# Optimization experiments

Hardware: AMD Instinct MI355X
Metric: run time of the kernel (lower is better)

## Reference

```python
import jax, jax.numpy as jnp
import numpy as np

H, W, D = 160, 160, 16
VOXEL_SIZE = 0.4
VOL_MIN = np.array([-32.0, -32.0, -1.0], dtype=np.float32)
SCALE_MULTIPLIER = 3.0
N_GAUSS = 8192
CHUNK = 64


def setup_inputs() -> dict:
    key = jax.random.key(0)
    k1, k2, k3, k4, k5 = jax.random.split(key, 5)
    vol_min = jnp.asarray(VOL_MIN)
    vol_ext = jnp.array([64.0, 64.0, 6.4], dtype=jnp.float32)
    means3d = jax.random.uniform(k1, (N_GAUSS, 3), jnp.float32) * vol_ext + vol_min
    opacities = jax.random.uniform(k2, (N_GAUSS, 1), jnp.float32)
    # per-axis std devs: 0.2..0.8 m so 3-sigma footprint spans a handful of voxels
    scales = 0.2 + 0.6 * jax.random.uniform(k3, (N_GAUSS, 3), jnp.float32)
    rotations = jax.random.normal(k4, (N_GAUSS, 4), jnp.float32)
    features = jax.random.normal(k5, (N_GAUSS, 32), jnp.float32)
    return {"means3d": means3d, "opacities": opacities, "scales": scales,
            "rotations": rotations, "features": features}


def quat_to_rotmat(q):
    # q: [N,4] wxyz, normalized
    w, x, y, z = q[:, 0], q[:, 1], q[:, 2], q[:, 3]
    R = jnp.stack([
        jnp.stack([1 - 2 * (y * y + z * z), 2 * (x * y - w * z), 2 * (x * z + w * y)], -1),
        jnp.stack([2 * (x * y + w * z), 1 - 2 * (x * x + z * z), 2 * (y * z - w * x)], -1),
        jnp.stack([2 * (x * z - w * y), 2 * (y * z + w * x), 1 - 2 * (x * x + y * y)], -1),
    ], axis=-2)  # [N,3,3]
    return R


def _grid_coords():
    ii, jj, kk = jnp.meshgrid(jnp.arange(H), jnp.arange(W), jnp.arange(D), indexing="ij")
    idx = jnp.stack([ii, jj, kk], axis=-1).astype(jnp.float32)
    return (idx + 0.5) * VOXEL_SIZE + jnp.asarray(VOL_MIN)  # [H,W,D,3] voxel centers


def reference(means3d, opacities, scales, rotations, features):
    x = _grid_coords().reshape(-1, 3)  # [V,3]
    q = rotations / jnp.linalg.norm(rotations, axis=-1, keepdims=True)
    R = quat_to_rotmat(q)
    # covariance = R diag(s^2) R^T
    cov = jnp.einsum("nij,nj,nkj->nik", R, scales * scales, R)
    cov_inv = jnp.linalg.inv(cov)
    sigma = jnp.sqrt(jnp.diagonal(cov, axis1=1, axis2=2))  # [N,3]
    opac = opacities[:, 0]  # [N]
    n = means3d.shape[0]
    nchunks = n // CHUNK

    def chunked(a):
        return a.reshape(nchunks, CHUNK, *a.shape[1:])

    def step(acc, c):
        mu, op, sg, ci, ft = c
        diff = x[:, None, :] - mu[None, :, :]  # [V,CHUNK,3]
        maha = jnp.einsum("vci,cij,vcj->vc", diff, ci, diff)
        # local aggregation cutoff: within scale_multiplier * sigma box around mean
        mask = jnp.all(jnp.abs(diff) <= SCALE_MULTIPLIER * sg[None, :, :], axis=-1)
        w = op[None, :] * jnp.exp(-0.5 * maha) * mask  # [V,CHUNK]
        return acc + w @ ft, None

    acc0 = jnp.zeros((x.shape[0], features.shape[-1]), jnp.float32)
    xs = (chunked(means3d), chunked(opac), chunked(sigma), chunked(cov_inv), chunked(features))
    acc, _ = jax.lax.scan(step, acc0, xs)
    return acc.reshape(H, W, D, features.shape[-1])
```

## Files before the change

kernel.cpp:

```cpp
#include <hip/hip_runtime.h>

#define HH 160
#define WW 160
#define DD 16
#define NG 8192
#define VOXEL 0.4f

#define TTX 20
#define TTY 20
#define TTZ 4
#define NTILES (TTX * TTY * TTZ)
#define CAP 128


__global__ __launch_bounds__(64) void gv_precompute_bin(
    const float* __restrict__ means, const float* __restrict__ opac,
    const float* __restrict__ scales, const float* __restrict__ rots,
    const float4* __restrict__ feats, int* __restrict__ tileCnt,
    float4* __restrict__ tileData) {
  int g = blockIdx.x * 64 + threadIdx.x;
  if (g >= NG) return;
  float qw = rots[g * 4 + 0], qx = rots[g * 4 + 1];
  float qy = rots[g * 4 + 2], qz = rots[g * 4 + 3];
  float inv = rsqrtf(qw * qw + qx * qx + qy * qy + qz * qz);
  qw *= inv; qx *= inv; qy *= inv; qz *= inv;
  float R[3][3];
  R[0][0] = 1.f - 2.f * (qy * qy + qz * qz);
  R[0][1] = 2.f * (qx * qy - qw * qz);
  R[0][2] = 2.f * (qx * qz + qw * qy);
  R[1][0] = 2.f * (qx * qy + qw * qz);
  R[1][1] = 1.f - 2.f * (qx * qx + qz * qz);
  R[1][2] = 2.f * (qy * qz - qw * qx);
  R[2][0] = 2.f * (qx * qz - qw * qy);
  R[2][1] = 2.f * (qy * qz + qw * qx);
  R[2][2] = 1.f - 2.f * (qx * qx + qy * qy);
  float sx = scales[g * 3 + 0], sy = scales[g * 3 + 1], sz = scales[g * 3 + 2];
  float s2[3] = {sx * sx, sy * sy, sz * sz};
  float is2[3] = {1.f / s2[0], 1.f / s2[1], 1.f / s2[2]};
  float cov00 = 0.f, cov11 = 0.f, cov22 = 0.f;
  float ci00 = 0.f, ci01 = 0.f, ci02 = 0.f, ci11 = 0.f, ci12 = 0.f, ci22 = 0.f;
#pragma unroll
  for (int c = 0; c < 3; c++) {
    cov00 += R[0][c] * R[0][c] * s2[c];
    cov11 += R[1][c] * R[1][c] * s2[c];
    cov22 += R[2][c] * R[2][c] * s2[c];
    ci00 += R[0][c] * R[0][c] * is2[c];
    ci01 += R[0][c] * R[1][c] * is2[c];
    ci02 += R[0][c] * R[2][c] * is2[c];
    ci11 += R[1][c] * R[1][c] * is2[c];
    ci12 += R[1][c] * R[2][c] * is2[c];
    ci22 += R[2][c] * R[2][c] * is2[c];
  }
  float mx = means[g * 3 + 0], my = means[g * 3 + 1], mz = means[g * 3 + 2];
  float bx = 3.f * sqrtf(cov00), by = 3.f * sqrtf(cov11), bz = 3.f * sqrtf(cov22);

  const float eps = 1e-4f;
  int i0 = (int)ceilf((mx - bx + 32.f) * 2.5f - 0.5f - eps);
  int i1 = (int)floorf((mx + bx + 32.f) * 2.5f - 0.5f + eps);
  int j0 = (int)ceilf((my - by + 32.f) * 2.5f - 0.5f - eps);
  int j1 = (int)floorf((my + by + 32.f) * 2.5f - 0.5f + eps);
  int k0 = (int)ceilf((mz - bz + 1.f) * 2.5f - 0.5f - eps);
  int k1 = (int)floorf((mz + bz + 1.f) * 2.5f - 0.5f + eps);
  i0 = max(i0, 0); i1 = min(i1, HH - 1);
  j0 = max(j0, 0); j1 = min(j1, WW - 1);
  k0 = max(k0, 0); k1 = min(k1, DD - 1);
  if (i0 > i1 || j0 > j1 || k0 > k1) return;

  float4 p0 = make_float4(mx, my, mz, opac[g]);
  float4 p1 = make_float4(bx, by, bz, ci00);
  float4 p2 = make_float4(ci01, ci02, ci11, ci12);
  float4 p3 = make_float4(ci22, 0.f, 0.f, 0.f);
  const float4* __restrict__ fsrc = feats + (size_t)g * 8;
  float4 f0 = fsrc[0], f1 = fsrc[1], f2 = fsrc[2], f3 = fsrc[3];
  float4 f4 = fsrc[4], f5 = fsrc[5], f6 = fsrc[6], f7 = fsrc[7];

  int ti0 = i0 >> 3, ti1 = i1 >> 3;
  int tj0 = j0 >> 3, tj1 = j1 >> 3;
  int tk0 = k0 >> 2, tk1 = k1 >> 2;
  for (int ti = ti0; ti <= ti1; ti++)
    for (int tj = tj0; tj <= tj1; tj++)
      for (int tk = tk0; tk <= tk1; tk++) {
        int t = (ti * TTY + tj) * TTZ + tk;
        int pos = atomicAdd(&tileCnt[t], 1);
        if (pos < CAP) {
          float4* __restrict__ d = tileData + ((size_t)t * CAP + pos) * 12;
          d[0] = p0;  d[1] = p1;  d[2] = p2;  d[3] = p3;
          d[4] = f0;  d[5] = f1;  d[6] = f2;  d[7] = f3;
          d[8] = f4;  d[9] = f5;  d[10] = f6; d[11] = f7;
        }
      }
}

__global__ __launch_bounds__(256) void gv_voxelize(
    const int* __restrict__ tileCnt, const float4* __restrict__ tileData,
    float4* __restrict__ out) {
  int tid = threadIdx.x;
  int dk = tid & 3, dj = (tid >> 2) & 7, di = tid >> 5;
  int tk = blockIdx.x, tj = blockIdx.y, ti = blockIdx.z;
  int i = ti * 8 + di, j = tj * 8 + dj, k = tk * 4 + dk;

  float px = (i + 0.5f) * VOXEL - 32.f;
  float py = (j + 0.5f) * VOXEL - 32.f;
  float pz = (k + 0.5f) * VOXEL - 1.f;

  int t = (ti * TTY + tj) * TTZ + tk;
  int cnt = tileCnt[t];
  cnt = min(cnt, CAP);
  const float4* __restrict__ gd = tileData + (size_t)t * CAP * 12;

  float4 acc[8];
#pragma unroll
  for (int f = 0; f < 8; f++) acc[f] = make_float4(0.f, 0.f, 0.f, 0.f);

  int n = 0;
  for (; n + 2 <= cnt; n += 2) {
    const float4* __restrict__ q0 = gd + (size_t)n * 12;
    const float4* __restrict__ q1 = q0 + 12;
    float4 a0 = q0[0], b0 = q0[1], c0 = q0[2], d0 = q0[3];
    float4 e00 = q0[4], e01 = q0[5], e02 = q0[6], e03 = q0[7];
    float4 e04 = q0[8], e05 = q0[9], e06 = q0[10], e07 = q0[11];
    float4 a1 = q1[0], b1 = q1[1], c1 = q1[2], d1 = q1[3];
    float4 e10 = q1[4], e11 = q1[5], e12 = q1[6], e13 = q1[7];
    float4 e14 = q1[8], e15 = q1[9], e16 = q1[10], e17 = q1[11];

    float dx0 = px - a0.x, dy0 = py - a0.y, dz0 = pz - a0.z;
    float dx1 = px - a1.x, dy1 = py - a1.y, dz1 = pz - a1.z;
    bool in0 = (fabsf(dx0) <= b0.x) & (fabsf(dy0) <= b0.y) & (fabsf(dz0) <= b0.z);
    bool in1 = (fabsf(dx1) <= b1.x) & (fabsf(dy1) <= b1.y) & (fabsf(dz1) <= b1.z);

    if (__any(in0)) {
      float maha = b0.w * dx0 * dx0 + c0.z * dy0 * dy0 + d0.x * dz0 * dz0 +
                   2.f * (c0.x * dx0 * dy0 + c0.y * dx0 * dz0 + c0.w * dy0 * dz0);
      float wgt = in0 ? a0.w * __expf(-0.5f * maha) : 0.f;
      acc[0].x += wgt * e00.x; acc[0].y += wgt * e00.y; acc[0].z += wgt * e00.z; acc[0].w += wgt * e00.w;
      acc[1].x += wgt * e01.x; acc[1].y += wgt * e01.y; acc[1].z += wgt * e01.z; acc[1].w += wgt * e01.w;
      acc[2].x += wgt * e02.x; acc[2].y += wgt * e02.y; acc[2].z += wgt * e02.z; acc[2].w += wgt * e02.w;
      acc[3].x += wgt * e03.x; acc[3].y += wgt * e03.y; acc[3].z += wgt * e03.z; acc[3].w += wgt * e03.w;
      acc[4].x += wgt * e04.x; acc[4].y += wgt * e04.y; acc[4].z += wgt * e04.z; acc[4].w += wgt * e04.w;
      acc[5].x += wgt * e05.x; acc[5].y += wgt * e05.y; acc[5].z += wgt * e05.z; acc[5].w += wgt * e05.w;
      acc[6].x += wgt * e06.x; acc[6].y += wgt * e06.y; acc[6].z += wgt * e06.z; acc[6].w += wgt * e06.w;
      acc[7].x += wgt * e07.x; acc[7].y += wgt * e07.y; acc[7].z += wgt * e07.z; acc[7].w += wgt * e07.w;
    }
    if (__any(in1)) {
      float maha = b1.w * dx1 * dx1 + c1.z * dy1 * dy1 + d1.x * dz1 * dz1 +
                   2.f * (c1.x * dx1 * dy1 + c1.y * dx1 * dz1 + c1.w * dy1 * dz1);
      float wgt = in1 ? a1.w * __expf(-0.5f * maha) : 0.f;
      acc[0].x += wgt * e10.x; acc[0].y += wgt * e10.y; acc[0].z += wgt * e10.z; acc[0].w += wgt * e10.w;
      acc[1].x += wgt * e11.x; acc[1].y += wgt * e11.y; acc[1].z += wgt * e11.z; acc[1].w += wgt * e11.w;
      acc[2].x += wgt * e12.x; acc[2].y += wgt * e12.y; acc[2].z += wgt * e12.z; acc[2].w += wgt * e12.w;
      acc[3].x += wgt * e13.x; acc[3].y += wgt * e13.y; acc[3].z += wgt * e13.z; acc[3].w += wgt * e13.w;
      acc[4].x += wgt * e14.x; acc[4].y += wgt * e14.y; acc[4].z += wgt * e14.z; acc[4].w += wgt * e14.w;
      acc[5].x += wgt * e15.x; acc[5].y += wgt * e15.y; acc[5].z += wgt * e15.z; acc[5].w += wgt * e15.w;
      acc[6].x += wgt * e16.x; acc[6].y += wgt * e16.y; acc[6].z += wgt * e16.z; acc[6].w += wgt * e16.w;
      acc[7].x += wgt * e17.x; acc[7].y += wgt * e17.y; acc[7].z += wgt * e17.z; acc[7].w += wgt * e17.w;
    }
  }
  if (n < cnt) {
    const float4* __restrict__ q = gd + (size_t)n * 12;
    float4 pa = q[0], pb = q[1], pc = q[2], pd = q[3];
    float dx = px - pa.x, dy = py - pa.y, dz = pz - pa.z;
    bool in = (fabsf(dx) <= pb.x) & (fabsf(dy) <= pb.y) & (fabsf(dz) <= pb.z);
    if (__any(in)) {
      float maha = pb.w * dx * dx + pc.z * dy * dy + pd.x * dz * dz +
                   2.f * (pc.x * dx * dy + pc.y * dx * dz + pc.w * dy * dz);
      float wgt = in ? pa.w * __expf(-0.5f * maha) : 0.f;
#pragma unroll
      for (int f = 0; f < 8; f++) {
        float4 fv = q[4 + f];
        acc[f].x += wgt * fv.x;
        acc[f].y += wgt * fv.y;
        acc[f].z += wgt * fv.z;
        acc[f].w += wgt * fv.w;
      }
    }
  }

  size_t v = ((size_t)i * WW + j) * DD + k;
  float4* o = out + v * 8;
#pragma unroll
  for (int f = 0; f < 8; f++) o[f] = acc[f];
}

extern "C" void kernel_launch(void* const* d_in, const int* in_sizes, int n_in,
                              void* d_out, int out_size, void* d_ws, size_t ws_size,
                              hipStream_t stream) {
  const float* means  = (const float*)d_in[0];
  const float* opac   = (const float*)d_in[1];
  const float* scales = (const float*)d_in[2];
  const float* rots   = (const float*)d_in[3];
  const float4* feats = (const float4*)d_in[4];

  char* ws = (char*)d_ws;
  int* tileCnt     = (int*)ws;
  float4* tileData = (float4*)(ws + 64 * 1024);

  hipMemsetAsync(tileCnt, 0, NTILES * sizeof(int), stream);
  gv_precompute_bin<<<128, 64, 0, stream>>>(means, opac, scales, rots,
                                            feats, tileCnt, tileData);
  dim3 grid(TTZ, TTY, TTX);
  gv_voxelize<<<grid, 256, 0, stream>>>(tileCnt, tileData, (float4*)d_out);
}
```

Baseline: 144.2 us.

## Bin compact gaussian params with index; gather features and stage params in LDS

The binning kernel now writes only 64 bytes of gaussian parameters per tile entry, with the gaussian index packed into a spare slot, instead of also copying 128 bytes of features. The voxelize kernel first stages the tile's parameter list into shared memory. It then reads features directly from the original feature array using a wave-uniform index. This reduces write traffic and scattered copies in binning and shrinks per-tile reads, at the cost of an extra indirection and a block barrier.

Measured after the change: 124.6 us. 1.16x faster.

```diff
diff --git a/kernel.cpp b/kernel.cpp
--- a/kernel.cpp
+++ b/kernel.cpp
@@ -16,8 +16,7 @@
 __global__ __launch_bounds__(64) void gv_precompute_bin(
     const float* __restrict__ means, const float* __restrict__ opac,
     const float* __restrict__ scales, const float* __restrict__ rots,
-    const float4* __restrict__ feats, int* __restrict__ tileCnt,
-    float4* __restrict__ tileData) {
+    int* __restrict__ tileCnt, float4* __restrict__ tilePack) {
   int g = blockIdx.x * 64 + threadIdx.x;
   if (g >= NG) return;
   float qw = rots[g * 4 + 0], qx = rots[g * 4 + 1];
@@ -69,10 +68,7 @@
   float4 p0 = make_float4(mx, my, mz, opac[g]);
   float4 p1 = make_float4(bx, by, bz, ci00);
   float4 p2 = make_float4(ci01, ci02, ci11, ci12);
-  float4 p3 = make_float4(ci22, 0.f, 0.f, 0.f);
-  const float4* __restrict__ fsrc = feats + (size_t)g * 8;
-  float4 f0 = fsrc[0], f1 = fsrc[1], f2 = fsrc[2], f3 = fsrc[3];
-  float4 f4 = fsrc[4], f5 = fsrc[5], f6 = fsrc[6], f7 = fsrc[7];
+  float4 p3 = make_float4(ci22, __int_as_float(g), 0.f, 0.f);
 
   int ti0 = i0 >> 3, ti1 = i1 >> 3;
   int tj0 = j0 >> 3, tj1 = j1 >> 3;
@@ -83,17 +79,17 @@
         int t = (ti * TTY + tj) * TTZ + tk;
         int pos = atomicAdd(&tileCnt[t], 1);
         if (pos < CAP) {
-          float4* __restrict__ d = tileData + ((size_t)t * CAP + pos) * 12;
+          float4* __restrict__ d = tilePack + ((size_t)t * CAP + pos) * 4;
           d[0] = p0;  d[1] = p1;  d[2] = p2;  d[3] = p3;
-          d[4] = f0;  d[5] = f1;  d[6] = f2;  d[7] = f3;
-          d[8] = f4;  d[9] = f5;  d[10] = f6; d[11] = f7;
         }
       }
 }
 
 __global__ __launch_bounds__(256) void gv_voxelize(
-    const int* __restrict__ tileCnt, const float4* __restrict__ tileData,
-    float4* __restrict__ out) {
+    const float4* __restrict__ feats, const int* __restrict__ tileCnt,
+    const float4* __restrict__ tilePack, float4* __restrict__ out) {
+  __shared__ float4 s_pack[CAP * 4];
+
   int tid = threadIdx.x;
   int dk = tid & 3, dj = (tid >> 2) & 7, di = tid >> 5;
   int tk = blockIdx.x, tj = blockIdx.y, ti = blockIdx.z;
@@ -106,7 +102,13 @@
   int t = (ti * TTY + tj) * TTZ + tk;
   int cnt = tileCnt[t];
   cnt = min(cnt, CAP);
-  const float4* __restrict__ gd = tileData + (size_t)t * CAP * 12;
+
+  {
+    const float4* __restrict__ src = tilePack + (size_t)t * CAP * 4;
+    int tot = cnt * 4;
+    for (int m = tid; m < tot; m += 256) s_pack[m] = src[m];
+  }
+  __syncthreads();
 
   float4 acc[8];
 #pragma unroll
@@ -114,14 +116,20 @@
 
   int n = 0;
   for (; n + 2 <= cnt; n += 2) {
-    const float4* __restrict__ q0 = gd + (size_t)n * 12;
-    const float4* __restrict__ q1 = q0 + 12;
-    float4 a0 = q0[0], b0 = q0[1], c0 = q0[2], d0 = q0[3];
-    float4 e00 = q0[4], e01 = q0[5], e02 = q0[6], e03 = q0[7];
-    float4 e04 = q0[8], e05 = q0[9], e06 = q0[10], e07 = q0[11];
-    float4 a1 = q1[0], b1 = q1[1], c1 = q1[2], d1 = q1[3];
-    float4 e10 = q1[4], e11 = q1[5], e12 = q1[6], e13 = q1[7];
-    float4 e14 = q1[8], e15 = q1[9], e16 = q1[10], e17 = q1[11];
+    float4 a0 = s_pack[n * 4 + 0], b0 = s_pack[n * 4 + 1];
+    float4 c0 = s_pack[n * 4 + 2], d0 = s_pack[n * 4 + 3];
+    float4 a1 = s_pack[n * 4 + 4], b1 = s_pack[n * 4 + 5];
+    float4 c1 = s_pack[n * 4 + 6], d1 = s_pack[n * 4 + 7];
+
+    int g0 = __builtin_amdgcn_readfirstlane(__float_as_int(d0.y));
+    int g1 = __builtin_amdgcn_readfirstlane(__float_as_int(d1.y));
+    const float4* __restrict__ fp0 = feats + (size_t)g0 * 8;
+    const float4* __restrict__ fp1 = feats + (size_t)g1 * 8;
+    float4 F0[8], F1[8];
+#pragma unroll
+    for (int f = 0; f < 8; f++) F0[f] = fp0[f];
+#pragma unroll
+    for (int f = 0; f < 8; f++) F1[f] = fp1[f];
 
     float dx0 = px - a0.x, dy0 = py - a0.y, dz0 = pz - a0.z;
     float dx1 = px - a1.x, dy1 = py - a1.y, dz1 = pz - a1.z;
@@ -132,32 +140,32 @@
       float maha = b0.w * dx0 * dx0 + c0.z * dy0 * dy0 + d0.x * dz0 * dz0 +
                    2.f * (c0.x * dx0 * dy0 + c0.y * dx0 * dz0 + c0.w * dy0 * dz0);
       float wgt = in0 ? a0.w * __expf(-0.5f * maha) : 0.f;
-      acc[0].x += wgt * e00.x; acc[0].y += wgt * e00.y; acc[0].z += wgt * e00.z; acc[0].w += wgt * e00.w;
-      acc[1].x += wgt * e01.x; acc[1].y += wgt * e01.y; acc[1].z += wgt * e01.z; acc[1].w += wgt * e01.w;
-      acc[2].x += wgt * e02.x; acc[2].y += wgt * e02.y; acc[2].z += wgt * e02.z; acc[2].w += wgt * e02.w;
-      acc[3].x += wgt * e03.x; acc[3].y += wgt * e03.y; acc[3].z += wgt * e03.z; acc[3].w += wgt * e03.w;
-      acc[4].x += wgt * e04.x; acc[4].y += wgt * e04.y; acc[4].z += wgt * e04.z; acc[4].w += wgt * e04.w;
-      acc[5].x += wgt * e05.x; acc[5].y += wgt * e05.y; acc[5].z += wgt * e05.z; acc[5].w += wgt * e05.w;
-      acc[6].x += wgt * e06.x; acc[6].y += wgt * e06.y; acc[6].z += wgt * e06.z; acc[6].w += wgt * e06.w;
-      acc[7].x += wgt * e07.x; acc[7].y += wgt * e07.y; acc[7].z += wgt * e07.z; acc[7].w += wgt * e07.w;
+#pragma unroll
+      for (int f = 0; f < 8; f++) {
+        acc[f].x += wgt * F0[f].x;
+        acc[f].y += wgt * F0[f].y;
+        acc[f].z += wgt * F0[f].z;
+        acc[f].w += wgt * F0[f].w;
+      }
     }
     if (__any(in1)) {
       float maha = b1.w * dx1 * dx1 + c1.z * dy1 * dy1 + d1.x * dz1 * dz1 +
                    2.f * (c1.x * dx1 * dy1 + c1.y * dx1 * dz1 + c1.w * dy1 * dz1);
       float wgt = in1 ? a1.w * __expf(-0.5f * maha) : 0.f;
-      acc[0].x += wgt * e10.x; acc[0].y += wgt * e10.y; acc[0].z += wgt * e10.z; acc[0].w += wgt * e10.w;
-      acc[1].x += wgt * e11.x; acc[1].y += wgt * e11.y; acc[1].z += wgt * e11.z; acc[1].w += wgt * e11.w;
-      acc[2].x += wgt * e12.x; acc[2].y += wgt * e12.y; acc[2].z += wgt * e12.z; acc[2].w += wgt * e12.w;
-      acc[3].x += wgt * e13.x; acc[3].y += wgt * e13.y; acc[3].z += wgt * e13.z; acc[3].w += wgt * e13.w;
-      acc[4].x += wgt * e14.x; acc[4].y += wgt * e14.y; acc[4].z += wgt * e14.z; acc[4].w += wgt * e14.w;
-      acc[5].x += wgt * e15.x; acc[5].y += wgt * e15.y; acc[5].z += wgt * e15.z; acc[5].w += wgt * e15.w;
-      acc[6].x += wgt * e16.x; acc[6].y += wgt * e16.y; acc[6].z += wgt * e16.z; acc[6].w += wgt * e16.w;
-      acc[7].x += wgt * e17.x; acc[7].y += wgt * e17.y; acc[7].z += wgt * e17.z; acc[7].w += wgt * e17.w;
+#pragma unroll
+      for (int f = 0; f < 8; f++) {
+        acc[f].x += wgt * F1[f].x;
+        acc[f].y += wgt * F1[f].y;
+        acc[f].z += wgt * F1[f].z;
+        acc[f].w += wgt * F1[f].w;
+      }
     }
   }
   if (n < cnt) {
-    const float4* __restrict__ q = gd + (size_t)n * 12;
-    float4 pa = q[0], pb = q[1], pc = q[2], pd = q[3];
+    float4 pa = s_pack[n * 4 + 0], pb = s_pack[n * 4 + 1];
+    float4 pc = s_pack[n * 4 + 2], pd = s_pack[n * 4 + 3];
+    int gg = __builtin_amdgcn_readfirstlane(__float_as_int(pd.y));
+    const float4* __restrict__ fp = feats + (size_t)gg * 8;
     float dx = px - pa.x, dy = py - pa.y, dz = pz - pa.z;
     bool in = (fabsf(dx) <= pb.x) & (fabsf(dy) <= pb.y) & (fabsf(dz) <= pb.z);
     if (__any(in)) {
@@ -166,7 +174,7 @@
       float wgt = in ? pa.w * __expf(-0.5f * maha) : 0.f;
 #pragma unroll
       for (int f = 0; f < 8; f++) {
-        float4 fv = q[4 + f];
+        float4 fv = fp[f];
         acc[f].x += wgt * fv.x;
         acc[f].y += wgt * fv.y;
         acc[f].z += wgt * fv.z;
@@ -192,11 +200,12 @@
 
   char* ws = (char*)d_ws;
   int* tileCnt     = (int*)ws;
-  float4* tileData = (float4*)(ws + 64 * 1024);
+  float4* tilePack = (float4*)(ws + 64 * 1024);
 
   hipMemsetAsync(tileCnt, 0, NTILES * sizeof(int), stream);
   gv_precompute_bin<<<128, 64, 0, stream>>>(means, opac, scales, rots,
-                                            feats, tileCnt, tileData);
+                                            tileCnt, tilePack);
   dim3 grid(TTZ, TTY, TTX);
-  gv_voxelize<<<grid, 256, 0, stream>>>(tileCnt, tileData, (float4*)d_out);
+  gv_voxelize<<<grid, 256, 0, stream>>>(feats, tileCnt, tilePack,
+                                        (float4*)d_out);
 }
```
